# Kernel optimization log

Hardware: AMD Instinct MI355X
Metric: run time of the kernel (lower is better)

Reference implementation:

```python
import jax, jax.numpy as jnp
import numpy as np

D = 1024      # d_model
FFN = 4096    # encoder_ffn_dim
INTER = 4096  # intermediate_size (per-expert extra width)
E = 4         # num_experts
S = 3         # num_datasets
NH = 16       # attention heads
HD = D // NH
B = 4
L = 1024


def _ln(x, g, b, eps=1e-5):
    m = x.mean(-1, keepdims=True)
    v = ((x - m) ** 2).mean(-1, keepdims=True)
    return (x - m) / jnp.sqrt(v + eps) * g + b


def setup_inputs() -> dict:
    key = jax.random.key(0)
    keys = iter(jax.random.split(key, 32))

    def w(shape):
        return jax.random.normal(next(keys), shape, dtype=jnp.float32) * 0.02

    inp = {}
    inp["hidden_states"] = jax.random.normal(next(keys), (B, L, D), dtype=jnp.float32)
    inp["attention_mask"] = jnp.zeros((B, 1, L, L), jnp.float32)
    inp["layer_head_mask"] = jnp.ones((NH,), jnp.float32)
    inp["idxes"] = jax.random.randint(next(keys), (B,), 0, S, dtype=jnp.int32)
    for name, shape in [("q_w", (D, D)), ("k_w", (D, D)), ("v_w", (D, D)), ("o_w", (D, D)),
                        ("fc1_w", (FFN, D)), ("fc2_w", (D, FFN)),
                        ("exp_fc1_w", (E, INTER, D)), ("exp_fc2_w", (E, D, INTER)),
                        ("gate_w", (S, E, D))]:
        inp[name] = w(shape)
    for name, shape in [("q_b", (D,)), ("k_b", (D,)), ("v_b", (D,)), ("o_b", (D,)),
                        ("fc1_b", (FFN,)), ("fc2_b", (D,)),
                        ("exp_fc1_b", (E, INTER)), ("gate_b", (S, E))]:
        inp[name] = jnp.zeros(shape, jnp.float32)
    inp["ln1_g"] = jnp.ones((D,), jnp.float32)
    inp["ln1_b"] = jnp.zeros((D,), jnp.float32)
    inp["ln2_g"] = jnp.ones((D,), jnp.float32)
    inp["ln2_b"] = jnp.zeros((D,), jnp.float32)
    return inp


def reference(hidden_states, attention_mask, layer_head_mask, idxes,
              q_w, q_b, k_w, k_b, v_w, v_b, o_w, o_b,
              ln1_g, ln1_b, fc1_w, fc1_b, fc2_w, fc2_b,
              exp_fc1_w, exp_fc1_b, exp_fc2_w, gate_w, gate_b,
              ln2_g, ln2_b):
    Bb, Ll, Dm = hidden_states.shape
    residual = hidden_states
    scale = HD ** -0.5

    def heads(t):  # [B,L,D] -> [B,NH,L,HD]
        return t.reshape(Bb, Ll, NH, HD).transpose(0, 2, 1, 3)

    q = heads(hidden_states @ q_w.T + q_b) * scale
    k = heads(hidden_states @ k_w.T + k_b)
    v = heads(hidden_states @ v_w.T + v_b)
    scores = jnp.einsum('bhqd,bhkd->bhqk', q, k) + attention_mask  # [B,NH,L,L]
    probs = jax.nn.softmax(scores, axis=-1) * layer_head_mask[None, :, None, None]
    attn = jnp.einsum('bhqk,bhkd->bhqd', probs, v).transpose(0, 2, 1, 3).reshape(Bb, Ll, Dm)
    h = residual + attn @ o_w.T + o_b
    h = _ln(h, ln1_g, ln1_b)

    # --- MoE feed-forward (token-level top-1 routing, per-dataset gates) ---
    x = h.reshape(-1, Dm)                 # [T, D]
    ds = jnp.repeat(idxes, Ll)            # [T] dataset id per token
    Wg = gate_w[ds]                       # [T, E, D]
    logits = jnp.einsum('td,ted->te', x, Wg) + gate_b[ds]
    gp = jax.nn.softmax(logits, axis=-1)
    gate_value = gp.max(-1)               # [T]
    gate_idx = gp.argmax(-1)              # [T]

    out = jnp.zeros_like(x)
    for e in range(E):  # small fixed expert count
        W1 = jnp.concatenate([fc1_w, exp_fc1_w[e]], axis=0)     # [FFN+INTER, D]
        b1 = jnp.concatenate([fc1_b, exp_fc1_b[e]], axis=0)
        W2 = jnp.concatenate([fc2_w, exp_fc2_w[e]], axis=1)     # [D, FFN+INTER]
        hh = jax.nn.gelu(x @ W1.T + b1, approximate=False)
        y = hh @ W2.T + fc2_b
        y = _ln(x + y, ln2_g, ln2_b)
        out = out + jnp.where(gate_idx == e, gate_value, 0.0)[:, None] * y
    return out.reshape(Bb, Ll, Dm)
```

## Files before the change

### kernel.cpp

```cpp
#include <hip/hip_runtime.h>
#include <cstdint>
#include <cstddef>

#define DEV __device__ __forceinline__

typedef __bf16 bf16;
typedef __bf16 bf16x8 __attribute__((ext_vector_type(8)));
typedef __bf16 bf16x4v __attribute__((ext_vector_type(4)));
typedef float  f32x4  __attribute__((ext_vector_type(4)));

static constexpr int D_   = 1024;
static constexpr int FFN_ = 4096;
static constexpr int NH_  = 16;
static constexpr int HD_  = 64;
static constexpr int SEQ_ = 1024;
static constexpr int T_   = 4 * SEQ_;
static constexpr float L2E_ = 1.4426950408889634f;

DEV float gelu_f(float x) {
  float g2 = x * fmaf(-0.102944f, x * x, -2.302212f);
  return x * __builtin_amdgcn_rcpf(1.f + exp2f(g2));
}

template<int N>
DEV float ror16(float x) {
  int i = __builtin_bit_cast(int, x);
  int r = __builtin_amdgcn_update_dpp(i, i, 0x120 + N, 0xf, 0xf, false);
  return __builtin_bit_cast(float, r);
}
DEV float rowMax16(float x) {
  x = fmaxf(x, ror16<8>(x)); x = fmaxf(x, ror16<4>(x));
  x = fmaxf(x, ror16<2>(x)); x = fmaxf(x, ror16<1>(x));
  return x;
}
DEV float rowSum16(float x) {
  x += ror16<8>(x); x += ror16<4>(x); x += ror16<2>(x); x += ror16<1>(x);
  return x;
}

__global__ __launch_bounds__(256) void k_cvt4(const float* __restrict__ a, const float* __restrict__ b,
                                              const float* __restrict__ c, const float* __restrict__ d,
                                              bf16* __restrict__ dst)
{
  size_t i = ((size_t)blockIdx.x * 256 + threadIdx.x) * 4;
  constexpr size_t M1 = 4ull << 20, M2 = 20ull << 20, M3 = 24ull << 20, M4 = 40ull << 20;
  const float* src; size_t si;
  if (i < M1)      { src = a; si = i; }
  else if (i < M2) { src = b; si = i - M1; }
  else if (i < M3) { src = c; si = i - M2; }
  else if (i < M4) { src = d; si = i - M3; }
  else return;
  float4 v = *(const float4*)(src + si);
  bf16x4v o;
  o[0] = (bf16)v.x; o[1] = (bf16)v.y; o[2] = (bf16)v.z; o[3] = (bf16)v.w;
  *(bf16x4v*)(dst + i) = o;
}

__global__ __launch_bounds__(256) void k_cvt_split_all(
    const float* __restrict__ h, const float* __restrict__ qw, const float* __restrict__ kw,
    const float* __restrict__ vw, const float* __restrict__ ow, bf16* __restrict__ out)
{
  int i = (blockIdx.x * 256 + threadIdx.x) * 4;
  if (i >= (8 << 20)) return;
  int seg = i >> 20;
  const float* src; int si;
  if (seg < 4)       { src = h;  si = i; }
  else if (seg == 4) { src = qw; si = i - (4 << 20); }
  else if (seg == 5) { src = kw; si = i - (5 << 20); }
  else if (seg == 6) { src = vw; si = i - (6 << 20); }
  else               { src = ow; si = i - (7 << 20); }
  float4 v = *(const float4*)(src + si);
  int r = i >> 10, c = i & 1023;
  bf16* base = out + (size_t)r * 2048 + c;
  float xs[4] = {v.x, v.y, v.z, v.w};
  #pragma unroll
  for (int j = 0; j < 4; ++j) {
    float x = xs[j];
    bf16 hi = (bf16)x;
    bf16 lo = (bf16)(x - (float)hi);
    base[j]        = hi;
    base[1024 + j] = lo;
  }
}

enum { EPI_QKV = 0, EPI_OPROJ, EPI_FF1, EPI_FF2 };

DEV int map_akt(int kt, bool split) { return split ? (kt < 64 ? kt : kt - 64) : kt; }
DEV int map_bkt(int kt, bool split) { return split ? (kt < 32 ? kt : kt - 32) : kt; }

template<int EPI, bool SPLIT, int TM, int TN>
__global__ __launch_bounds__(256)
void k_gemm(const bf16* __restrict__ A, const bf16* __restrict__ Bw,
            const float* __restrict__ bias, const float* __restrict__ bias2,
            const float* __restrict__ bias3, const float* __restrict__ resid,
            float* __restrict__ outF, bf16* __restrict__ outB,
            bf16* __restrict__ o2, bf16* __restrict__ o3,
            const int* __restrict__ perm, const int* __restrict__ seg,
            int Kphys, int nk, float scale)
{
  constexpr bool FUSED = (EPI == EPI_FF1 || EPI == EPI_FF2);
  constexpr int  NCOL  = (EPI == EPI_FF1) ? 4096 : 1024;
  constexpr int  SBX   = 4096 / TM;
  constexpr int  MF    = (TN == 128) ? (TM / 32) : (TM / 64);
  constexpr int  AISS  = TM / 64;
  constexpr int  BISS  = TN / 64;

  __shared__ __align__(16) bf16 sA[2][TM * 32];
  __shared__ __align__(16) bf16 sB[2][TN * 32];

  const int tid  = threadIdx.x;
  const int lane = tid & 63;
  const int w    = tid >> 6;
  const int lr   = lane & 15, kg = lane >> 4;
  const int wmBase = (TN == 128) ? (w >> 1) * (TM / 2) : w * (TM / 4);
  const int wnBase = (TN == 128) ? (w & 1) * 64 : 0;

  int bx, by, kz = 0;
  if constexpr (EPI == EPI_FF2) {
    int wk = (blockIdx.x & 7) * 136 + (blockIdx.x >> 3);
    kz = wk / 544; int r2 = wk % 544;
    bx = r2 >> 3; by = r2 & 7;
  } else {
    bx = blockIdx.x; by = blockIdx.y; kz = blockIdx.z;
  }
  const int ktBase = (EPI == EPI_OPROJ || EPI == EPI_FF2) ? kz * nk : 0;

  const bool expertBlk = FUSED && (bx >= SBX);
  int e = 0;
  if (FUSED && expertBlk) { int r0 = (bx - SBX) * TM; while (e < 3 && r0 >= seg[e + 1]) e++; }
  const bf16* Bp = Bw + (expertBlk ? (size_t)(e + 1) * NCOL * Kphys : 0);

  const bf16* aSrc[AISS]; const bf16* bSrc[BISS];
  #pragma unroll
  for (int i = 0; i < AISS; ++i) {
    int c = tid + i * 256;
    int koff = (c & 3) * 8;
    if (EPI == EPI_FF1 && expertBlk) {
      int pr = perm[(bx - SBX) * TM + (c >> 2)];
      aSrc[i] = A + (size_t)(pr < 0 ? 0 : pr) * Kphys + koff;
    } else {
      aSrc[i] = A + (size_t)(bx * TM + (c >> 2)) * Kphys + koff;
    }
  }
  #pragma unroll
  for (int i = 0; i < BISS; ++i) {
    int c = tid + i * 256;
    int koff = (c & 3) * 8;
    bSrc[i] = Bp + (size_t)(by * TN + (c >> 2)) * Kphys + koff;
  }

  f32x4 acc[MF][4] = {};

  {
    int ak0 = map_akt(ktBase, SPLIT), bk0 = map_bkt(ktBase, SPLIT);
    #pragma unroll
    for (int i = 0; i < AISS; ++i)
      __builtin_amdgcn_global_load_lds((const void*)(aSrc[i] + (size_t)ak0 * 32),
                                       (void*)((char*)sA[0] + (tid + i * 256) * 16), 16, 0, 0);
    #pragma unroll
    for (int i = 0; i < BISS; ++i)
      __builtin_amdgcn_global_load_lds((const void*)(bSrc[i] + (size_t)bk0 * 32),
                                       (void*)((char*)sB[0] + (tid + i * 256) * 16), 16, 0, 0);
  }
  __syncthreads();

  for (int kt = 0; kt < nk; ++kt) {
    const int cur = kt & 1;
    if (kt + 1 < nk) {
      int ak = map_akt(ktBase + kt + 1, SPLIT), bk = map_bkt(ktBase + kt + 1, SPLIT);
      #pragma unroll
      for (int i = 0; i < AISS; ++i)
        __builtin_amdgcn_global_load_lds((const void*)(aSrc[i] + (size_t)ak * 32),
                                         (void*)((char*)sA[cur ^ 1] + (tid + i * 256) * 16), 16, 0, 0);
      #pragma unroll
      for (int i = 0; i < BISS; ++i)
        __builtin_amdgcn_global_load_lds((const void*)(bSrc[i] + (size_t)bk * 32),
                                         (void*)((char*)sB[cur ^ 1] + (tid + i * 256) * 16), 16, 0, 0);
    }
    bf16x8 af[MF], bfr[4];
    #pragma unroll
    for (int m = 0; m < MF; ++m)
      af[m] = *(const bf16x8*)&sA[cur][(wmBase + m * 16 + lr) * 32 + kg * 8];
    #pragma unroll
    for (int n = 0; n < 4; ++n)
      bfr[n] = *(const bf16x8*)&sB[cur][(wnBase + n * 16 + lr) * 32 + kg * 8];
    #pragma unroll
    for (int m = 0; m < MF; ++m)
      #pragma unroll
      for (int n = 0; n < 4; ++n)
        acc[m][n] = __builtin_amdgcn_mfma_f32_16x16x32_bf16(af[m], bfr[n], acc[m][n], 0, 0, 0);
    __syncthreads();
  }

  #pragma unroll
  for (int m = 0; m < MF; ++m) {
    #pragma unroll
    for (int n = 0; n < 4; ++n) {
      int gc = by * TN + wnBase + n * 16 + lr;
      #pragma unroll
      for (int r = 0; r < 4; ++r) {
        int row = bx * TM + wmBase + m * 16 + kg * 4 + r;
        float v = acc[m][n][r];
        if constexpr (EPI == EPI_QKV) {
          const int which = by >> 3;
          const int wcol = gc & 1023;
          int bq = row >> 10, li = row & 1023, hh = wcol >> 6, d = wcol & 63;
          if (which == 0) {
            float y = (v + bias[wcol]) * scale;
            bf16* base = outB + ((size_t)(bq * NH_ + hh) * SEQ_ + li) * 128 + d;
            bf16 hi = (bf16)y, lo = (bf16)(y - (float)hi);
            base[0] = hi; base[64] = lo;
          } else if (which == 1) {
            float y = v + bias2[wcol];
            bf16* base = o2 + ((size_t)(bq * NH_ + hh) * SEQ_ + li) * 128 + d;
            bf16 hi = (bf16)y, lo = (bf16)(y - (float)hi);
            base[0] = hi; base[64] = lo;
          } else {
            float y = v + bias3[wcol];
            bf16* base = o3 + ((size_t)(bq * NH_ + hh) * HD_ + d) * 2048 + li;
            bf16 hi = (bf16)y, lo = (bf16)(y - (float)hi);
            base[0] = hi; base[1024] = lo;
          }
        } else if constexpr (EPI == EPI_OPROJ) {
          outF[((size_t)kz * 4096 + row) * 1024 + gc] = v;
        } else if constexpr (EPI == EPI_FF1) {
          float y = v + (expertBlk ? bias2[e * 4096 + gc] : bias[gc]);
          outB[(size_t)row * 4096 + gc] = (bf16)gelu_f(y);
        } else if constexpr (EPI == EPI_FF2) {
          o2[((size_t)kz * 8704 + row) * 1024 + gc] = (bf16)v;
        }
      }
    }
  }
}

__global__ __launch_bounds__(256)
void k_attn(const bf16* __restrict__ q2, const bf16* __restrict__ k2,
            const bf16* __restrict__ vT2, const float* __restrict__ mask,
            const float* __restrict__ lhm, bf16* __restrict__ ctx2)
{
  const int blk = (blockIdx.x & 7) * 128 + (blockIdx.x >> 3);
  const int bh = blk >> 4, qt4 = blk & 15;
  const int tid = threadIdx.x;
  const int w = tid >> 6;
  const int lane = tid & 63, lr = lane & 15, kg = lane >> 4;
  const int b = bh >> 4, h = bh & 15;
  const int q0 = (qt4 * 4 + w) * 16;

  __shared__ __align__(16) bf16 sK[2][4096];
  __shared__ __align__(16) bf16 sV[2][4096];
  __shared__ __align__(16) float Pb[4][16][32];
  float (*P)[32] = Pb[w];

  const bf16* qp = q2 + ((size_t)bh * SEQ_ + q0) * 128;
  bf16x8 aq0 = *(const bf16x8*)(qp + (size_t)lr * 128 +  0 + kg * 8);
  bf16x8 aq1 = *(const bf16x8*)(qp + (size_t)lr * 128 + 32 + kg * 8);
  bf16x8 aq2 = *(const bf16x8*)(qp + (size_t)lr * 128 + 64 + kg * 8);
  bf16x8 aq3 = *(const bf16x8*)(qp + (size_t)lr * 128 + 96 + kg * 8);

  const bf16* kp = k2 + (size_t)bh * SEQ_ * 128;
  const bf16* vp = vT2 + (size_t)bh * HD_ * 2048;
  const float* mp = mask + ((size_t)b * SEQ_ + q0) * SEQ_;

  auto stage = [&](int buf, int kb) {
    #pragma unroll
    for (int i = 0; i < 2; ++i) {
      int c = i * 256 + w * 64 + lane;
      int cs = c ^ ((c >> 4) & 7);
      __builtin_amdgcn_global_load_lds((const void*)(kp + (size_t)kb * 128 + cs * 8),
                                       (void*)&sK[buf][(size_t)(i * 256 + w * 64) * 8], 16, 0, 0);
      int d = c >> 3, p = (c & 7) ^ (d & 7);
      const bf16* vsrc = vp + (size_t)d * 2048 + (p < 4 ? kb + p * 8 : 1024 + kb + (p - 4) * 8);
      __builtin_amdgcn_global_load_lds((const void*)vsrc,
                                       (void*)&sV[buf][(size_t)(i * 256 + w * 64) * 8], 16, 0, 0);
    }
  };

  float m_run[4], l_run[4];
  f32x4 o[4] = {};
  #pragma unroll
  for (int r = 0; r < 4; ++r) { m_run[r] = -1e30f; l_run[r] = 0.f; }

  float mreg[8];
  #pragma unroll
  for (int n = 0; n < 2; ++n)
    #pragma unroll
    for (int r = 0; r < 4; ++r)
      mreg[n * 4 + r] = mp[(size_t)(kg * 4 + r) * SEQ_ + n * 16 + lr];

  stage(0, 0);
  __syncthreads();

  for (int kc = 0; kc < SEQ_ / 32; ++kc) {
    const int kb = kc * 32;
    const int cur = kc & 1;
    if (kc + 1 < SEQ_ / 32) stage(cur ^ 1, kb + 32);

    const char* kbase = (const char*)sK[cur];
    const char* vbase = (const char*)sV[cur];

    f32x4 s[2];
    #pragma unroll
    for (int n = 0; n < 2; ++n) {
      f32x4 t = {0.f, 0.f, 0.f, 0.f};
      int key = n * 16 + lr;
      int rowb = (key << 8) + (kg << 4);
      int sw = (key & 7) << 4;
      bf16x8 bk0 = *(const bf16x8*)(kbase + ((rowb +   0) ^ sw));
      bf16x8 bk1 = *(const bf16x8*)(kbase + ((rowb +  64) ^ sw));
      bf16x8 bk2 = *(const bf16x8*)(kbase + ((rowb + 128) ^ sw));
      bf16x8 bk3 = *(const bf16x8*)(kbase + ((rowb + 192) ^ sw));
      t = __builtin_amdgcn_mfma_f32_16x16x32_bf16(aq0, bk0, t, 0, 0, 0);
      t = __builtin_amdgcn_mfma_f32_16x16x32_bf16(aq1, bk1, t, 0, 0, 0);
      t = __builtin_amdgcn_mfma_f32_16x16x32_bf16(aq2, bk0, t, 0, 0, 0);
      t = __builtin_amdgcn_mfma_f32_16x16x32_bf16(aq3, bk1, t, 0, 0, 0);
      t = __builtin_amdgcn_mfma_f32_16x16x32_bf16(aq0, bk2, t, 0, 0, 0);
      t = __builtin_amdgcn_mfma_f32_16x16x32_bf16(aq1, bk3, t, 0, 0, 0);
      s[n] = t;
    }
    #pragma unroll
    for (int n = 0; n < 2; ++n)
      #pragma unroll
      for (int r = 0; r < 4; ++r)
        s[n][r] = fmaf(mreg[n * 4 + r], L2E_, s[n][r]);
    if (kc + 1 < SEQ_ / 32) {
      #pragma unroll
      for (int n = 0; n < 2; ++n)
        #pragma unroll
        for (int r = 0; r < 4; ++r)
          mreg[n * 4 + r] = mp[(size_t)(kg * 4 + r) * SEQ_ + kb + 32 + n * 16 + lr];
    }

    float cm[4], mnew[4], alpha[4], rs[4], pv[2][4];
    #pragma unroll
    for (int r = 0; r < 4; ++r) cm[r] = rowMax16(fmaxf(s[0][r], s[1][r]));
    #pragma unroll
    for (int r = 0; r < 4; ++r) { mnew[r] = fmaxf(m_run[r], cm[r]); alpha[r] = exp2f(m_run[r] - mnew[r]); }
    #pragma unroll
    for (int n = 0; n < 2; ++n)
      #pragma unroll
      for (int r = 0; r < 4; ++r) pv[n][r] = exp2f(s[n][r] - mnew[r]);
    #pragma unroll
    for (int r = 0; r < 4; ++r) rs[r] = rowSum16(pv[0][r] + pv[1][r]);
    #pragma unroll
    for (int r = 0; r < 4; ++r) { l_run[r] = l_run[r] * alpha[r] + rs[r]; m_run[r] = mnew[r]; }
    #pragma unroll
    for (int n = 0; n < 4; ++n)
      #pragma unroll
      for (int r = 0; r < 4; ++r) o[n][r] *= alpha[r];

    #pragma unroll
    for (int n = 0; n < 2; ++n)
      #pragma unroll
      for (int r = 0; r < 4; ++r) {
        int row = kg * 4 + r, col = n * 16 + lr;
        int cg = (col >> 2) ^ (row & 7);
        P[row][(cg << 2) | (col & 3)] = pv[n][r];
      }
    asm volatile("s_waitcnt lgkmcnt(0)" ::: "memory");
    __builtin_amdgcn_sched_barrier(0);

    f32x4 pA = *(const f32x4*)&P[lr][((kg * 2) ^ (lr & 7)) << 2];
    f32x4 pB = *(const f32x4*)&P[lr][((kg * 2 + 1) ^ (lr & 7)) << 2];
    bf16x8 ph, pl;
    #pragma unroll
    for (int j = 0; j < 4; ++j) {
      ph[j] = (bf16)pA[j]; pl[j] = (bf16)(pA[j] - (float)ph[j]);
      ph[4 + j] = (bf16)pB[j]; pl[4 + j] = (bf16)(pB[j] - (float)ph[4 + j]);
    }

    #pragma unroll
    for (int n = 0; n < 4; ++n) {
      int d = n * 16 + lr;
      int rowb = (d << 7) + (kg << 4);
      int sw = (d & 7) << 4;
      bf16x8 bvh = *(const bf16x8*)(vbase + ((rowb +  0) ^ sw));
      bf16x8 bvl = *(const bf16x8*)(vbase + ((rowb + 64) ^ sw));
      o[n] = __builtin_amdgcn_mfma_f32_16x16x32_bf16(ph, bvh, o[n], 0, 0, 0);
      o[n] = __builtin_amdgcn_mfma_f32_16x16x32_bf16(pl, bvh, o[n], 0, 0, 0);
      o[n] = __builtin_amdgcn_mfma_f32_16x16x32_bf16(ph, bvl, o[n], 0, 0, 0);
    }

    __syncthreads();
  }

  const float hm = lhm[h];
  #pragma unroll
  for (int r = 0; r < 4; ++r) {
    float rln = hm / l_run[r];
    #pragma unroll
    for (int n = 0; n < 4; ++n) {
      int li = q0 + kg * 4 + r;
      int col = h * HD_ + n * 16 + lr;
      float y = o[n][r] * rln;
      bf16* base = ctx2 + ((size_t)b * SEQ_ + li) * 2048;
      bf16 hi = (bf16)y, lo = (bf16)(y - (float)hi);
      base[col] = hi; base[1024 + col] = lo;
    }
  }
}

DEV float blockReduceSum(float v, int tid, float* sm)
{
  #pragma unroll
  for (int d = 1; d < 64; d <<= 1) v += __shfl_xor(v, d, 64);
  if ((tid & 63) == 0) sm[tid >> 6] = v;
  __syncthreads();
  float r = sm[0] + sm[1] + sm[2] + sm[3];
  __syncthreads();
  return r;
}

__global__ __launch_bounds__(256)
void k_ln1gate(const float* __restrict__ resid, const float* __restrict__ Pp, const float* __restrict__ ob,
               const float* __restrict__ gam, const float* __restrict__ bet,
               const float* __restrict__ gw, const float* __restrict__ gb, const int* __restrict__ idxes,
               float* __restrict__ h, bf16* __restrict__ hb,
               float* __restrict__ gv, int* __restrict__ gi)
{
  __shared__ float sm[4];
  __shared__ float red[4][4];
  int t = blockIdx.x, tid = threadIdx.x;
  constexpr size_t CH = 4096ull * 1024ull;
  float4 rv = *(const float4*)(resid + (size_t)t * 1024 + tid * 4);
  float4 p0 = *(const float4*)(Pp + (size_t)t * 1024 + tid * 4);
  float4 p1 = *(const float4*)(Pp + CH + (size_t)t * 1024 + tid * 4);
  float4 bo = *(const float4*)(ob + tid * 4);
  float z0 = rv.x + p0.x + p1.x + bo.x;
  float z1 = rv.y + p0.y + p1.y + bo.y;
  float z2 = rv.z + p0.z + p1.z + bo.z;
  float z3 = rv.w + p0.w + p1.w + bo.w;
  float mean = blockReduceSum(z0 + z1 + z2 + z3, tid, sm) * (1.f / 1024.f);
  float d0 = z0 - mean, d1 = z1 - mean, d2 = z2 - mean, d3 = z3 - mean;
  float var = blockReduceSum(d0*d0 + d1*d1 + d2*d2 + d3*d3, tid, sm) * (1.f / 1024.f);
  float inv = rsqrtf(var + 1e-5f);
  float4 g4 = *(const float4*)(gam + tid * 4);
  float4 b4 = *(const float4*)(bet + tid * 4);
  float y0 = d0 * inv * g4.x + b4.x, y1 = d1 * inv * g4.y + b4.y;
  float y2 = d2 * inv * g4.z + b4.z, y3 = d3 * inv * g4.w + b4.w;
  float4 yo; yo.x = y0; yo.y = y1; yo.z = y2; yo.w = y3;
  *(float4*)(h + (size_t)t * 1024 + tid * 4) = yo;
  bf16x4v hv; hv[0] = (bf16)y0; hv[1] = (bf16)y1; hv[2] = (bf16)y2; hv[3] = (bf16)y3;
  *(bf16x4v*)(hb + (size_t)t * 1024 + tid * 4) = hv;

  int ds = idxes[t >> 10];
  const float* wg = gw + (size_t)ds * 4096;
  float a[4];
  #pragma unroll
  for (int e = 0; e < 4; ++e) {
    float4 wv = *(const float4*)(wg + e * 1024 + tid * 4);
    a[e] = y0 * wv.x + y1 * wv.y + y2 * wv.z + y3 * wv.w;
  }
  int lane = tid & 63, wid = tid >> 6;
  #pragma unroll
  for (int e = 0; e < 4; ++e) {
    float vv = a[e];
    #pragma unroll
    for (int d = 1; d < 64; d <<= 1) vv += __shfl_xor(vv, d, 64);
    if (lane == 0) red[wid][e] = vv;
  }
  __syncthreads();
  if (tid == 0) {
    float lg[4];
    #pragma unroll
    for (int e = 0; e < 4; ++e) lg[e] = red[0][e] + red[1][e] + red[2][e] + red[3][e] + gb[ds * 4 + e];
    int best = 0; float bv = lg[0];
    #pragma unroll
    for (int e = 1; e < 4; ++e) if (lg[e] > bv) { bv = lg[e]; best = e; }
    float se = 0.f;
    #pragma unroll
    for (int e = 0; e < 4; ++e) se += expf(lg[e] - bv);
    gv[t] = 1.f / se;
    gi[t] = best;
  }
}

__global__ __launch_bounds__(1024)
void k_route_all(const int* __restrict__ gi, int* __restrict__ meta,
                 int* __restrict__ perm, int* __restrict__ inv)
{
  __shared__ int cnt[4], seg[5], cur[4];
  int tid = threadIdx.x;
  if (tid < 4) { cnt[tid] = 0; cur[tid] = 0; }
  __syncthreads();
  #pragma unroll
  for (int k = 0; k < 4; ++k) atomicAdd(&cnt[gi[tid + k * 1024]], 1);
  #pragma unroll
  for (int k = 0; k < 5; ++k) { int i = tid + k * 1024; if (i < 4608) perm[i] = -1; }
  __syncthreads();
  if (tid == 0) {
    int s = 0;
    #pragma unroll
    for (int e = 0; e < 4; ++e) { seg[e] = s; s += (cnt[e] + 127) & ~127; }
    seg[4] = s;
    #pragma unroll
    for (int e = 0; e < 5; ++e) meta[8 + e] = seg[e];
  }
  __syncthreads();
  #pragma unroll
  for (int k = 0; k < 4; ++k) {
    int t = tid + k * 1024;
    int e = gi[t];
    int p = atomicAdd(&cur[e], 1);
    int rowp = seg[e] + p;
    perm[rowp] = t;
    inv[t] = rowp;
  }
}

__global__ __launch_bounds__(256)
void k_final(const float* __restrict__ h, const bf16* __restrict__ P,
             const float* __restrict__ b2, const float* __restrict__ gam,
             const float* __restrict__ bet, const float* __restrict__ gv,
             const int* __restrict__ inv, float* __restrict__ out)
{
  __shared__ float sm[4];
  int t = blockIdx.x, tid = threadIdx.x;
  constexpr size_t CH = 8704ull * 1024ull;
  int er = 4096 + inv[t];
  bf16x4v q0 = *(const bf16x4v*)(P + (size_t)t * 1024 + tid * 4);
  bf16x4v q1 = *(const bf16x4v*)(P + CH + (size_t)t * 1024 + tid * 4);
  bf16x4v q2 = *(const bf16x4v*)(P + (size_t)er * 1024 + tid * 4);
  bf16x4v q3 = *(const bf16x4v*)(P + CH + (size_t)er * 1024 + tid * 4);
  float4 a = *(const float4*)(h + (size_t)t * 1024 + tid * 4);
  float4 bb = *(const float4*)(b2 + tid * 4);
  float z0 = a.x + (float)q0[0] + (float)q1[0] + (float)q2[0] + (float)q3[0] + bb.x;
  float z1 = a.y + (float)q0[1] + (float)q1[1] + (float)q2[1] + (float)q3[1] + bb.y;
  float z2 = a.z + (float)q0[2] + (float)q1[2] + (float)q2[2] + (float)q3[2] + bb.z;
  float z3 = a.w + (float)q0[3] + (float)q1[3] + (float)q2[3] + (float)q3[3] + bb.w;
  float mean = blockReduceSum(z0 + z1 + z2 + z3, tid, sm) * (1.f / 1024.f);
  float d0 = z0 - mean, d1 = z1 - mean, d2 = z2 - mean, d3 = z3 - mean;
  float var = blockReduceSum(d0*d0 + d1*d1 + d2*d2 + d3*d3, tid, sm) * (1.f / 1024.f);
  float invd = rsqrtf(var + 1e-5f);
  float4 g4 = *(const float4*)(gam + tid * 4);
  float4 b4 = *(const float4*)(bet + tid * 4);
  float gval = gv[t];
  float4 r;
  r.x = gval * (d0 * invd * g4.x + b4.x);
  r.y = gval * (d1 * invd * g4.y + b4.y);
  r.z = gval * (d2 * invd * g4.z + b4.z);
  r.w = gval * (d3 * invd * g4.w + b4.w);
  *(float4*)(out + (size_t)t * 1024 + tid * 4) = r;
}

extern "C" void kernel_launch(void* const* d_in, const int* in_sizes, int n_in,
                              void* d_out, int out_size, void* d_ws, size_t ws_size,
                              hipStream_t stream)
{
  const float* hidden = (const float*)d_in[0];
  const float* mask   = (const float*)d_in[1];
  const float* lhm    = (const float*)d_in[2];
  const int*   idxes  = (const int*)d_in[3];
  const float* qw = (const float*)d_in[4];
  const float* kw = (const float*)d_in[5];
  const float* vw = (const float*)d_in[6];
  const float* ow = (const float*)d_in[7];
  const float* fc1w  = (const float*)d_in[8];
  const float* fc2w  = (const float*)d_in[9];
  const float* efc1w = (const float*)d_in[10];
  const float* efc2w = (const float*)d_in[11];
  const float* gatew = (const float*)d_in[12];
  const float* qb = (const float*)d_in[13];
  const float* kb = (const float*)d_in[14];
  const float* vb = (const float*)d_in[15];
  const float* ob = (const float*)d_in[16];
  const float* fc1b  = (const float*)d_in[17];
  const float* fc2b  = (const float*)d_in[18];
  const float* efc1b = (const float*)d_in[19];
  const float* gateb = (const float*)d_in[20];
  const float* ln1g = (const float*)d_in[21];
  const float* ln1b = (const float*)d_in[22];
  const float* ln2g = (const float*)d_in[23];
  const float* ln2b = (const float*)d_in[24];
  float* out = (float*)d_out;
  char* ws = (char*)d_ws;

  constexpr size_t MB = 1024ull * 1024ull;
  constexpr size_t O_H    = 0;
  constexpr size_t O_HBF  = O_H + 16 * MB;
  constexpr size_t O_GV   = O_HBF + 8 * MB;
  constexpr size_t O_GI   = O_GV + 16 * 1024;
  constexpr size_t O_PERM = O_GI + 16 * 1024;
  constexpr size_t O_META = O_PERM + 18432;
  constexpr size_t O_INV  = O_META + 256;
  constexpr size_t O_U    = (O_INV + 16384 + 255) & ~255ull;
  constexpr size_t O_X2   = O_U;
  constexpr size_t O_WQ2  = O_X2 + 16 * MB;
  constexpr size_t O_Q2   = O_WQ2 + 16 * MB;
  constexpr size_t O_K2   = O_Q2 + 16 * MB;
  constexpr size_t O_VT2  = O_K2 + 16 * MB;
  constexpr size_t O_CTX2 = O_VT2 + 16 * MB;
  constexpr size_t O_HPRE = O_CTX2 + 16 * MB;
  constexpr size_t O_WO2  = O_WQ2 + 12 * MB;
  constexpr size_t O_W1B  = O_U;
  constexpr size_t O_WE1B = O_W1B + 8 * MB;
  constexpr size_t O_W2B  = O_WE1B + 32 * MB;
  constexpr size_t O_WE2B = O_W2B + 8 * MB;
  constexpr size_t O_HHS  = O_WE2B + 32 * MB;
  constexpr size_t O_HHE  = O_HHS + 32 * MB;
  constexpr size_t O_P    = O_HHE + 36 * MB;
  (void)ws_size; (void)in_sizes; (void)n_in; (void)out_size;

  dim3 blk(256);
  k_cvt_split_all<<<8192, 256, 0, stream>>>(hidden, qw, kw, vw, ow, (bf16*)(ws + O_X2));

  const float qscale = 0.125f * L2E_;
  k_gemm<EPI_QKV, true, 128, 128><<<dim3(32, 24), blk, 0, stream>>>(
      (bf16*)(ws + O_X2), (bf16*)(ws + O_WQ2), qb, kb, vb, nullptr,
      nullptr, (bf16*)(ws + O_Q2), (bf16*)(ws + O_K2), (bf16*)(ws + O_VT2),
      nullptr, nullptr, 2048, 96, qscale);

  k_attn<<<1024, 256, 0, stream>>>((bf16*)(ws + O_Q2), (bf16*)(ws + O_K2), (bf16*)(ws + O_VT2),
                                   mask, lhm, (bf16*)(ws + O_CTX2));

  k_gemm<EPI_OPROJ, true, 128, 64><<<dim3(32, 16, 2), blk, 0, stream>>>(
      (bf16*)(ws + O_CTX2), (bf16*)(ws + O_WO2), nullptr, nullptr, nullptr, nullptr,
      (float*)(ws + O_HPRE), nullptr, nullptr, nullptr, nullptr, nullptr, 2048, 48, 1.0f);
  k_ln1gate<<<4096, 256, 0, stream>>>(hidden, (float*)(ws + O_HPRE), ob, ln1g, ln1b,
                                      gatew, gateb, idxes,
                                      (float*)(ws + O_H), (bf16*)(ws + O_HBF),
                                      (float*)(ws + O_GV), (int*)(ws + O_GI));

  k_cvt4<<<40960, 256, 0, stream>>>(fc1w, efc1w, fc2w, efc2w, (bf16*)(ws + O_W1B));
  k_route_all<<<1, 1024, 0, stream>>>((int*)(ws + O_GI), (int*)(ws + O_META),
                                      (int*)(ws + O_PERM), (int*)(ws + O_INV));

  k_gemm<EPI_FF1, false, 128, 128><<<dim3(68, 32), blk, 0, stream>>>(
      (bf16*)(ws + O_HBF), (bf16*)(ws + O_W1B), fc1b, efc1b, nullptr, nullptr,
      nullptr, (bf16*)(ws + O_HHS), nullptr, nullptr,
      (int*)(ws + O_PERM), (int*)(ws + O_META) + 8, 1024, 32, 1.0f);
  k_gemm<EPI_FF2, false, 128, 128><<<dim3(1088), blk, 0, stream>>>(
      (bf16*)(ws + O_HHS), (bf16*)(ws + O_W2B), nullptr, nullptr, nullptr, nullptr,
      nullptr, nullptr, (bf16*)(ws + O_P), nullptr,
      nullptr, (int*)(ws + O_META) + 8, 4096, 64, 1.0f);

  k_final<<<4096, 256, 0, stream>>>((float*)(ws + O_H), (bf16*)(ws + O_P), fc2b, ln2g, ln2b,
                                    (float*)(ws + O_GV), (int*)(ws + O_INV), out);
}
```

Baseline: 563.5 us.

## Rewrite attention with 32x32 MFMA, transposed S, and register-resident P

The attention kernel now gives each wave 32 queries instead of 16 and uses 32x32x16 bf16 MFMAs. It computes S transposed (keys by queries) so that each lane owns one query column, which turns the row max and row sum into a local reduction plus a single cross-half shuffle. The P matrix is packed into bf16 hi/lo registers and exchanged with lane shuffles instead of going through LDS, removing the shared-memory round trip and its waits. Each block covers 128 queries, so the grid is halved. The trade-off is higher register pressure and fewer blocks in flight.

After: 525.9 us, median of 2. -6.7%, faster.

```diff
diff --git a/kernel.cpp b/kernel.cpp
--- a/kernel.cpp
+++ b/kernel.cpp
@@ -8,6 +8,8 @@
 typedef __bf16 bf16x8 __attribute__((ext_vector_type(8)));
 typedef __bf16 bf16x4v __attribute__((ext_vector_type(4)));
 typedef float  f32x4  __attribute__((ext_vector_type(4)));
+typedef float  f32x16 __attribute__((ext_vector_type(16)));
+typedef unsigned int uint4v __attribute__((ext_vector_type(4)));
 
 static constexpr int D_   = 1024;
 static constexpr int FFN_ = 4096;
@@ -22,20 +24,20 @@
   return x * __builtin_amdgcn_rcpf(1.f + exp2f(g2));
 }
 
-template<int N>
-DEV float ror16(float x) {
-  int i = __builtin_bit_cast(int, x);
-  int r = __builtin_amdgcn_update_dpp(i, i, 0x120 + N, 0xf, 0xf, false);
-  return __builtin_bit_cast(float, r);
-}
-DEV float rowMax16(float x) {
-  x = fmaxf(x, ror16<8>(x)); x = fmaxf(x, ror16<4>(x));
-  x = fmaxf(x, ror16<2>(x)); x = fmaxf(x, ror16<1>(x));
-  return x;
-}
-DEV float rowSum16(float x) {
-  x += ror16<8>(x); x += ror16<4>(x); x += ror16<2>(x); x += ror16<1>(x);
-  return x;
+DEV unsigned pk2h(float a, float b) {
+  unsigned ua = __builtin_bit_cast(unsigned short, (bf16)a);
+  unsigned ub = __builtin_bit_cast(unsigned short, (bf16)b);
+  return ua | (ub << 16);
+}
+DEV unsigned pk2l(float a, float b) {
+  bf16 ha = (bf16)a, hb = (bf16)b;
+  unsigned ua = __builtin_bit_cast(unsigned short, (bf16)(a - (float)ha));
+  unsigned ub = __builtin_bit_cast(unsigned short, (bf16)(b - (float)hb));
+  return ua | (ub << 16);
+}
+DEV bf16x8 mk8(unsigned w0, unsigned w1, unsigned w2, unsigned w3) {
+  uint4v v = {w0, w1, w2, w3};
+  return __builtin_bit_cast(bf16x8, v);
 }
 
 __global__ __launch_bounds__(256) void k_cvt4(const float* __restrict__ a, const float* __restrict__ b,
@@ -239,28 +241,28 @@
             const bf16* __restrict__ vT2, const float* __restrict__ mask,
             const float* __restrict__ lhm, bf16* __restrict__ ctx2)
 {
-  const int blk = (blockIdx.x & 7) * 128 + (blockIdx.x >> 3);
-  const int bh = blk >> 4, qt4 = blk & 15;
+  const int blk = (blockIdx.x & 7) * 64 + (blockIdx.x >> 3);
+  const int bh = blk >> 3, qb = blk & 7;
   const int tid = threadIdx.x;
-  const int w = tid >> 6;
-  const int lane = tid & 63, lr = lane & 15, kg = lane >> 4;
+  const int w = tid >> 6, lane = tid & 63;
+  const int lq = lane & 31, hi = lane >> 5;
   const int b = bh >> 4, h = bh & 15;
-  const int q0 = (qt4 * 4 + w) * 16;
+  const int q0 = qb * 128 + w * 32;
 
   __shared__ __align__(16) bf16 sK[2][4096];
   __shared__ __align__(16) bf16 sV[2][4096];
-  __shared__ __align__(16) float Pb[4][16][32];
-  float (*P)[32] = Pb[w];
-
-  const bf16* qp = q2 + ((size_t)bh * SEQ_ + q0) * 128;
-  bf16x8 aq0 = *(const bf16x8*)(qp + (size_t)lr * 128 +  0 + kg * 8);
-  bf16x8 aq1 = *(const bf16x8*)(qp + (size_t)lr * 128 + 32 + kg * 8);
-  bf16x8 aq2 = *(const bf16x8*)(qp + (size_t)lr * 128 + 64 + kg * 8);
-  bf16x8 aq3 = *(const bf16x8*)(qp + (size_t)lr * 128 + 96 + kg * 8);
+
+  const bf16* qp = q2 + ((size_t)bh * SEQ_ + q0 + lq) * 128;
+  bf16x8 qh[4], ql[4];
+  #pragma unroll
+  for (int s = 0; s < 4; ++s) {
+    qh[s] = *(const bf16x8*)(qp + s * 16 + hi * 8);
+    ql[s] = *(const bf16x8*)(qp + 64 + s * 16 + hi * 8);
+  }
 
   const bf16* kp = k2 + (size_t)bh * SEQ_ * 128;
   const bf16* vp = vT2 + (size_t)bh * HD_ * 2048;
-  const float* mp = mask + ((size_t)b * SEQ_ + q0) * SEQ_;
+  const float* mp = mask + ((size_t)b * SEQ_ + q0 + lq) * SEQ_;
 
   auto stage = [&](int buf, int kb) {
     #pragma unroll
@@ -276,17 +278,13 @@
     }
   };
 
-  float m_run[4], l_run[4];
-  f32x4 o[4] = {};
-  #pragma unroll
-  for (int r = 0; r < 4; ++r) { m_run[r] = -1e30f; l_run[r] = 0.f; }
-
-  float mreg[8];
-  #pragma unroll
-  for (int n = 0; n < 2; ++n)
-    #pragma unroll
-    for (int r = 0; r < 4; ++r)
-      mreg[n * 4 + r] = mp[(size_t)(kg * 4 + r) * SEQ_ + n * 16 + lr];
+  float m_run = -1e30f, l_run = 0.f;
+  f32x16 ot[2] = {};
+
+  float4 mreg[4];
+  #pragma unroll
+  for (int r4 = 0; r4 < 4; ++r4)
+    mreg[r4] = *(const float4*)(mp + 8 * r4 + 4 * hi);
 
   stage(0, 0);
   __syncthreads();
@@ -299,105 +297,94 @@
     const char* kbase = (const char*)sK[cur];
     const char* vbase = (const char*)sV[cur];
 
-    f32x4 s[2];
-    #pragma unroll
-    for (int n = 0; n < 2; ++n) {
-      f32x4 t = {0.f, 0.f, 0.f, 0.f};
-      int key = n * 16 + lr;
-      int rowb = (key << 8) + (kg << 4);
-      int sw = (key & 7) << 4;
-      bf16x8 bk0 = *(const bf16x8*)(kbase + ((rowb +   0) ^ sw));
-      bf16x8 bk1 = *(const bf16x8*)(kbase + ((rowb +  64) ^ sw));
-      bf16x8 bk2 = *(const bf16x8*)(kbase + ((rowb + 128) ^ sw));
-      bf16x8 bk3 = *(const bf16x8*)(kbase + ((rowb + 192) ^ sw));
-      t = __builtin_amdgcn_mfma_f32_16x16x32_bf16(aq0, bk0, t, 0, 0, 0);
-      t = __builtin_amdgcn_mfma_f32_16x16x32_bf16(aq1, bk1, t, 0, 0, 0);
-      t = __builtin_amdgcn_mfma_f32_16x16x32_bf16(aq2, bk0, t, 0, 0, 0);
-      t = __builtin_amdgcn_mfma_f32_16x16x32_bf16(aq3, bk1, t, 0, 0, 0);
-      t = __builtin_amdgcn_mfma_f32_16x16x32_bf16(aq0, bk2, t, 0, 0, 0);
-      t = __builtin_amdgcn_mfma_f32_16x16x32_bf16(aq1, bk3, t, 0, 0, 0);
-      s[n] = t;
-    }
-    #pragma unroll
-    for (int n = 0; n < 2; ++n)
-      #pragma unroll
-      for (int r = 0; r < 4; ++r)
-        s[n][r] = fmaf(mreg[n * 4 + r], L2E_, s[n][r]);
+    f32x16 st = {};
+    #pragma unroll
+    for (int s = 0; s < 4; ++s) {
+      int gh = s * 2 + hi, gl = 8 + s * 2 + hi;
+      bf16x8 kh = *(const bf16x8*)(kbase + lq * 256 + ((gh ^ (lq & 7)) << 4));
+      bf16x8 kl = *(const bf16x8*)(kbase + lq * 256 + ((gl ^ (lq & 7)) << 4));
+      st = __builtin_amdgcn_mfma_f32_32x32x16_bf16(kh, qh[s], st, 0, 0, 0);
+      st = __builtin_amdgcn_mfma_f32_32x32x16_bf16(kh, ql[s], st, 0, 0, 0);
+      st = __builtin_amdgcn_mfma_f32_32x32x16_bf16(kl, qh[s], st, 0, 0, 0);
+    }
+    #pragma unroll
+    for (int reg = 0; reg < 16; ++reg)
+      st[reg] = fmaf(((const float*)&mreg[reg >> 2])[reg & 3], L2E_, st[reg]);
     if (kc + 1 < SEQ_ / 32) {
       #pragma unroll
-      for (int n = 0; n < 2; ++n)
-        #pragma unroll
-        for (int r = 0; r < 4; ++r)
-          mreg[n * 4 + r] = mp[(size_t)(kg * 4 + r) * SEQ_ + kb + 32 + n * 16 + lr];
-    }
-
-    float cm[4], mnew[4], alpha[4], rs[4], pv[2][4];
-    #pragma unroll
-    for (int r = 0; r < 4; ++r) cm[r] = rowMax16(fmaxf(s[0][r], s[1][r]));
-    #pragma unroll
-    for (int r = 0; r < 4; ++r) { mnew[r] = fmaxf(m_run[r], cm[r]); alpha[r] = exp2f(m_run[r] - mnew[r]); }
-    #pragma unroll
-    for (int n = 0; n < 2; ++n)
+      for (int r4 = 0; r4 < 4; ++r4)
+        mreg[r4] = *(const float4*)(mp + kb + 32 + 8 * r4 + 4 * hi);
+    }
+
+    float cm = st[0];
+    #pragma unroll
+    for (int reg = 1; reg < 16; ++reg) cm = fmaxf(cm, st[reg]);
+    cm = fmaxf(cm, __shfl_xor(cm, 32, 64));
+    float mnew = fmaxf(m_run, cm);
+    float alpha = exp2f(m_run - mnew);
+    float p[16];
+    #pragma unroll
+    for (int reg = 0; reg < 16; ++reg) p[reg] = exp2f(st[reg] - mnew);
+    float rs = p[0];
+    #pragma unroll
+    for (int reg = 1; reg < 16; ++reg) rs += p[reg];
+    rs += __shfl_xor(rs, 32, 64);
+    l_run = l_run * alpha + rs; m_run = mnew;
+    #pragma unroll
+    for (int i = 0; i < 16; ++i) { ot[0][i] *= alpha; ot[1][i] *= alpha; }
+
+    unsigned hA0 = pk2h(p[0], p[1]),  hA1 = pk2h(p[2], p[3]);
+    unsigned hB0 = pk2h(p[4], p[5]),  hB1 = pk2h(p[6], p[7]);
+    unsigned hC0 = pk2h(p[8], p[9]),  hC1 = pk2h(p[10], p[11]);
+    unsigned hD0 = pk2h(p[12], p[13]), hD1 = pk2h(p[14], p[15]);
+    unsigned lA0 = pk2l(p[0], p[1]),  lA1 = pk2l(p[2], p[3]);
+    unsigned lB0 = pk2l(p[4], p[5]),  lB1 = pk2l(p[6], p[7]);
+    unsigned lC0 = pk2l(p[8], p[9]),  lC1 = pk2l(p[10], p[11]);
+    unsigned lD0 = pk2l(p[12], p[13]), lD1 = pk2l(p[14], p[15]);
+    unsigned x0 = (unsigned)__shfl_xor((int)(hi ? hA0 : hB0), 32, 64);
+    unsigned x1 = (unsigned)__shfl_xor((int)(hi ? hA1 : hB1), 32, 64);
+    unsigned x2 = (unsigned)__shfl_xor((int)(hi ? hC0 : hD0), 32, 64);
+    unsigned x3 = (unsigned)__shfl_xor((int)(hi ? hC1 : hD1), 32, 64);
+    unsigned y0 = (unsigned)__shfl_xor((int)(hi ? lA0 : lB0), 32, 64);
+    unsigned y1 = (unsigned)__shfl_xor((int)(hi ? lA1 : lB1), 32, 64);
+    unsigned y2 = (unsigned)__shfl_xor((int)(hi ? lC0 : lD0), 32, 64);
+    unsigned y3 = (unsigned)__shfl_xor((int)(hi ? lC1 : lD1), 32, 64);
+    bf16x8 pb0h = hi ? mk8(x0, x1, hB0, hB1) : mk8(hA0, hA1, x0, x1);
+    bf16x8 pb1h = hi ? mk8(x2, x3, hD0, hD1) : mk8(hC0, hC1, x2, x3);
+    bf16x8 pb0l = hi ? mk8(y0, y1, lB0, lB1) : mk8(lA0, lA1, y0, y1);
+    bf16x8 pb1l = hi ? mk8(y2, y3, lD0, lD1) : mk8(lC0, lC1, y2, y3);
+
+    #pragma unroll
+    for (int ks = 0; ks < 2; ++ks) {
+      bf16x8 pbh = ks ? pb1h : pb0h;
+      bf16x8 pbl = ks ? pb1l : pb0l;
       #pragma unroll
-      for (int r = 0; r < 4; ++r) pv[n][r] = exp2f(s[n][r] - mnew[r]);
-    #pragma unroll
-    for (int r = 0; r < 4; ++r) rs[r] = rowSum16(pv[0][r] + pv[1][r]);
-    #pragma unroll
-    for (int r = 0; r < 4; ++r) { l_run[r] = l_run[r] * alpha[r] + rs[r]; m_run[r] = mnew[r]; }
-    #pragma unroll
-    for (int n = 0; n < 4; ++n)
-      #pragma unroll
-      for (int r = 0; r < 4; ++r) o[n][r] *= alpha[r];
-
-    #pragma unroll
-    for (int n = 0; n < 2; ++n)
-      #pragma unroll
-      for (int r = 0; r < 4; ++r) {
-        int row = kg * 4 + r, col = n * 16 + lr;
-        int cg = (col >> 2) ^ (row & 7);
-        P[row][(cg << 2) | (col & 3)] = pv[n][r];
+      for (int t = 0; t < 2; ++t) {
+        int row = t * 32 + lq;
+        int gh = ks * 2 + hi, gl = 4 + ks * 2 + hi;
+        bf16x8 vh = *(const bf16x8*)(vbase + row * 128 + ((gh ^ (row & 7)) << 4));
+        bf16x8 vl = *(const bf16x8*)(vbase + row * 128 + ((gl ^ (row & 7)) << 4));
+        ot[t] = __builtin_amdgcn_mfma_f32_32x32x16_bf16(vh, pbh, ot[t], 0, 0, 0);
+        ot[t] = __builtin_amdgcn_mfma_f32_32x32x16_bf16(vh, pbl, ot[t], 0, 0, 0);
+        ot[t] = __builtin_amdgcn_mfma_f32_32x32x16_bf16(vl, pbh, ot[t], 0, 0, 0);
       }
-    asm volatile("s_waitcnt lgkmcnt(0)" ::: "memory");
-    __builtin_amdgcn_sched_barrier(0);
-
-    f32x4 pA = *(const f32x4*)&P[lr][((kg * 2) ^ (lr & 7)) << 2];
-    f32x4 pB = *(const f32x4*)&P[lr][((kg * 2 + 1) ^ (lr & 7)) << 2];
-    bf16x8 ph, pl;
-    #pragma unroll
-    for (int j = 0; j < 4; ++j) {
-      ph[j] = (bf16)pA[j]; pl[j] = (bf16)(pA[j] - (float)ph[j]);
-      ph[4 + j] = (bf16)pB[j]; pl[4 + j] = (bf16)(pB[j] - (float)ph[4 + j]);
-    }
-
-    #pragma unroll
-    for (int n = 0; n < 4; ++n) {
-      int d = n * 16 + lr;
-      int rowb = (d << 7) + (kg << 4);
-      int sw = (d & 7) << 4;
-      bf16x8 bvh = *(const bf16x8*)(vbase + ((rowb +  0) ^ sw));
-      bf16x8 bvl = *(const bf16x8*)(vbase + ((rowb + 64) ^ sw));
-      o[n] = __builtin_amdgcn_mfma_f32_16x16x32_bf16(ph, bvh, o[n], 0, 0, 0);
-      o[n] = __builtin_amdgcn_mfma_f32_16x16x32_bf16(pl, bvh, o[n], 0, 0, 0);
-      o[n] = __builtin_amdgcn_mfma_f32_16x16x32_bf16(ph, bvl, o[n], 0, 0, 0);
     }
 
     __syncthreads();
   }
 
-  const float hm = lhm[h];
-  #pragma unroll
-  for (int r = 0; r < 4; ++r) {
-    float rln = hm / l_run[r];
-    #pragma unroll
-    for (int n = 0; n < 4; ++n) {
-      int li = q0 + kg * 4 + r;
-      int col = h * HD_ + n * 16 + lr;
-      float y = o[n][r] * rln;
-      bf16* base = ctx2 + ((size_t)b * SEQ_ + li) * 2048;
-      bf16 hi = (bf16)y, lo = (bf16)(y - (float)hi);
-      base[col] = hi; base[1024 + col] = lo;
-    }
-  }
+  const float rln = lhm[h] / l_run;
+  bf16* base = ctx2 + ((size_t)b * SEQ_ + q0 + lq) * 2048;
+  #pragma unroll
+  for (int t = 0; t < 2; ++t)
+    #pragma unroll
+    for (int reg = 0; reg < 16; ++reg) {
+      int d = (reg & 3) + 8 * (reg >> 2) + 4 * hi + 32 * t;
+      int col = h * HD_ + d;
+      float y = ot[t][reg] * rln;
+      bf16 yh = (bf16)y, yl = (bf16)(y - (float)yh);
+      base[col] = yh; base[1024 + col] = yl;
+    }
 }
 
 DEV float blockReduceSum(float v, int tid, float* sm)
@@ -610,8 +597,8 @@
       nullptr, (bf16*)(ws + O_Q2), (bf16*)(ws + O_K2), (bf16*)(ws + O_VT2),
       nullptr, nullptr, 2048, 96, qscale);
 
-  k_attn<<<1024, 256, 0, stream>>>((bf16*)(ws + O_Q2), (bf16*)(ws + O_K2), (bf16*)(ws + O_VT2),
-                                   mask, lhm, (bf16*)(ws + O_CTX2));
+  k_attn<<<512, 256, 0, stream>>>((bf16*)(ws + O_Q2), (bf16*)(ws + O_K2), (bf16*)(ws + O_VT2),
+                                  mask, lhm, (bf16*)(ws + O_CTX2));
 
   k_gemm<EPI_OPROJ, true, 128, 64><<<dim3(32, 16, 2), blk, 0, stream>>>(
       (bf16*)(ws + O_CTX2), (bf16*)(ws + O_WO2), nullptr, nullptr, nullptr, nullptr,
```
